# Kernel tuning notes

Hardware: AMD Instinct MI355X
Metric: run time of the kernel (lower is better)

The kernel has to match this reference:

```python
import jax, jax.numpy as jnp
import numpy as np

T = 5       # fixed temporal factor in the original forward
HEADS = 8
DIM = 512
DIM_HEAD = 64
INNER = HEADS * DIM_HEAD  # 512 (must equal DIM for the masked scatter)


def setup_inputs() -> dict:
    key = jax.random.key(0)
    ks = jax.random.split(key, 8)
    bt, n = 40, 3137  # b=8, t=5; n-1 = 56*56 visual tokens
    x = jax.random.normal(ks[0], (bt, n, DIM), dtype=jnp.float32)
    mask = jax.random.randint(ks[1], (bt, 56, 56), 0, 2).astype(jnp.float32)
    s = 1.0 / np.sqrt(DIM)
    w_vq = jax.random.normal(ks[2], (DIM, INNER), dtype=jnp.float32) * s
    w_vkv = jax.random.normal(ks[3], (DIM, 2 * INNER), dtype=jnp.float32) * s
    w_aqkv = jax.random.normal(ks[4], (DIM, 3 * INNER), dtype=jnp.float32) * s
    w_out = jax.random.normal(ks[5], (INNER, DIM), dtype=jnp.float32) * s
    b_out = jnp.zeros((DIM,), dtype=jnp.float32)
    return {"x": x, "mask": mask, "w_vq": w_vq, "w_vkv": w_vkv,
            "w_aqkv": w_aqkv, "w_out": w_out, "b_out": b_out}


def reference(x, mask, w_vq, w_vkv, w_aqkv, w_out, b_out):
    bt, n, dim = x.shape
    b = bt // T
    nv = n - 1
    dh = DIM_HEAD
    scale = dh ** -0.5

    A = x[:, 0]        # (bt, dim) -- single 'action' token per frame
    V = x[:, 1:]       # (bt, nv, dim)
    m = mask.reshape(bt, nv, 1)

    aq, ak, av = jnp.split(A @ w_aqkv, 3, axis=-1)      # each (bt, INNER)
    vk, vv = jnp.split(V @ w_vkv, 2, axis=-1)           # each (bt, nv, INNER)
    vq = V @ w_vq                                        # (bt, nv, INNER)

    # --- A -> V cross attention: per batch, T A-queries over T*nv V keys ---
    qa = aq.reshape(b, T, HEADS, dh)
    Kv = vk.reshape(b, T * nv, HEADS, dh)
    Vv = vv.reshape(b, T * nv, HEADS, dh)
    av_dots = jnp.einsum('bqhd,bkhd->bhqk', qa, Kv) * scale
    av_attn = jax.nn.softmax(av_dots, axis=-1)
    av_o = jnp.einsum('bhqk,bkhd->bqhd', av_attn, Vv)   # (b, T, H, dh)
    a_out = av_o.reshape(bt, 1, INNER)

    # --- V -> A cross attention with block mask: every V token attends only
    # to its own batch's T A-tokens (the -inf block fill in the original) ---
    Qv = vq.reshape(b, T, nv, HEADS, dh)
    Ka = ak.reshape(b, T, HEADS, dh)
    Va = av.reshape(b, T, HEADS, dh)
    va_dots = jnp.einsum('bfnhd,bkhd->bhfnk', Qv, Ka) * scale
    va_attn = jax.nn.softmax(va_dots, axis=-1)          # softmax over T keys
    va_o = jnp.einsum('bhfnk,bkhd->bfnhd', va_attn, Va)
    v_full = va_o.reshape(bt, nv, INNER)

    # original: scatter attn out into V.clone() then * mask, under no_grad()
    # => masked positions get attention output, others V*0 = 0; detached.
    v_out = jax.lax.stop_gradient(v_full * m)

    out = jnp.concatenate([a_out, v_out], axis=1)       # (bt, n, INNER)
    return out @ w_out + b_out
```

## Files before the change

kernel.cpp:

```cpp
#include <hip/hip_runtime.h>

typedef unsigned short u16;
typedef unsigned int u32;
typedef __attribute__((ext_vector_type(8))) u16 u16x8;
typedef __attribute__((ext_vector_type(8))) __bf16 bf16x8;
typedef __attribute__((ext_vector_type(4))) float f32x4;

__device__ __forceinline__ float b2f(u16 u){ return __uint_as_float(((u32)u)<<16); }
__device__ __forceinline__ u16 f2b(float f){
  u32 b = __float_as_uint(f);
  return (u16)((b + 0x7fffu + ((b>>16)&1u))>>16);
}
__device__ __forceinline__ void gload16(const void* g, void* l){
  __builtin_amdgcn_global_load_lds((__attribute__((address_space(1))) void*)g,
                                   (__attribute__((address_space(3))) void*)l, 16, 0, 0);
}
__device__ __forceinline__ float wred_max(float v){
#pragma unroll
  for (int o=32;o>0;o>>=1) v = fmaxf(v, __shfl_xor(v,o));
  return v;
}
__device__ __forceinline__ float wred_sum(float v){
#pragma unroll
  for (int o=32;o>0;o>>=1) v += __shfl_xor(v,o);
  return v;
}


__global__ void k_pre(const float* __restrict__ x, const float* __restrict__ wvq,
                      const float* __restrict__ wvkv, const float* __restrict__ wout,
                      const float* __restrict__ waqkv,
                      u16* __restrict__ xb, u16* __restrict__ W1T,
                      u16* __restrict__ WoutT, float* __restrict__ aqkv){
  const int bid = blockIdx.x, tid = threadIdx.x;
  if (bid < 2048){
    const int stride = 2048*256;
    for (int i = bid*256 + tid; i < 8030720; i += stride){
      const float4* p = (const float4*)(x + (size_t)i*8);
      float4 a = p[0], b = p[1];
      u16x8 o;
      o[0]=f2b(a.x); o[1]=f2b(a.y); o[2]=f2b(a.z); o[3]=f2b(a.w);
      o[4]=f2b(b.x); o[5]=f2b(b.y); o[6]=f2b(b.z); o[7]=f2b(b.w);
      *(u16x8*)(xb + (size_t)i*8) = o;
    }
  } else if (bid < 6144){
    int id = (bid-2048)*256 + tid;
    if (id < 786432){
      int n = id >> 9, k = id & 511;
      float v;
      if (n < 512){
        v = wvq[k*512 + n];
      } else {
        int j = n - 512, h = j >> 7, r = j & 127;
        int c2 = (r < 64) ? (h*64 + r) : (512 + h*64 + (r - 64));
        v = wvkv[k*1024 + c2];
      }
      W1T[id] = f2b(v);
    } else {
      int j = id - 786432;
      int n = j >> 9, k = j & 511;
      WoutT[j] = f2b(wout[k*512 + n]);
    }
  } else {
    int id = (bid-6144)*256 + tid;
    int bt = id / 1536, c = id % 1536;
    const float* xr = x + (size_t)bt*3137*512;
    float s = 0.f;
    for (int k=0;k<512;k++) s += xr[k]*waqkv[k*1536+c];
    aqkv[id] = s;
  }
}

template<int FOUT>
__global__ __launch_bounds__(512, 2) void k_gemm256(
    const u16* __restrict__ A, const u16* __restrict__ BT,
    int M, int N, int K, int NX,
    u16* __restrict__ Cb, float* __restrict__ Cf, const float* __restrict__ bias)
{
  __shared__ __align__(16) char Ls[4][32768];
  const int tid = threadIdx.x;
  const int wid = tid >> 6, lane = tid & 63;
  const int nwg = gridDim.x, orig = blockIdx.x;
  const int q8 = nwg >> 3, r8 = nwg & 7;
  const int xc = orig & 7, sl = orig >> 3;
  const int work = (xc < r8 ? xc*(q8+1) : r8*(q8+1) + (xc-r8)*q8) + sl;
  const int m0 = (work / NX) * 256, n0 = (work % NX) * 256;
  const size_t K2 = (size_t)K * 2;
  const char* Ab = (const char*)A;
  const char* Bb = (const char*)BT;
  size_t asrc[2], bsrc[2];
  const int ad0 = wid*1024, ad1 = 8192 + wid*1024;
#pragma unroll
  for (int i=0;i<2;i++){
    int row = (i*8 + wid)*16 + (lane & 15);
    int koff = (lane >> 4) << 4;
    int ra = m0 + row; if (ra >= M) ra = M - 1;
    asrc[i] = (size_t)ra * K2 + koff;
    bsrc[i] = (size_t)(n0 + row) * K2 + koff;
  }
#define STAGE(s4, ks) { \
    size_t ko = (size_t)(ks) * 64; \
    gload16(Ab + asrc[0] + ko, Ls[s4] + ad0); \
    gload16(Ab + asrc[1] + ko, Ls[s4] + ad1); \
    gload16(Bb + bsrc[0] + ko, Ls[s4] + 16384 + ad0); \
    gload16(Bb + bsrc[1] + ko, Ls[s4] + 16384 + ad1); }

  f32x4 acc[8][4] = {};
  const int awb = (wid >> 2) * 8192;
  const int bwb = 16384 + (wid & 3) * 4096;
  const int NS = K >> 5;
  STAGE(0,0) STAGE(1,1) STAGE(2,2)
  for (int s = 0; s < NS; ++s){
    if (s + 2 < NS)      { asm volatile("s_waitcnt vmcnt(8)" ::: "memory"); }
    else if (s + 1 < NS) { asm volatile("s_waitcnt vmcnt(4)" ::: "memory"); }
    else                 { asm volatile("s_waitcnt vmcnt(0)" ::: "memory"); }
    __builtin_amdgcn_s_barrier();
    __builtin_amdgcn_sched_barrier(0);
    if (s + 3 < NS) STAGE((s+3)&3, s+3)
    const char* base = Ls[s & 3];
    bf16x8 af[8], bfr[4];
#pragma unroll
    for (int i=0;i<4;i++) af[i]  = *(const bf16x8*)(base + awb + i*1024 + lane*16);
#pragma unroll
    for (int i=0;i<4;i++) bfr[i] = *(const bf16x8*)(base + bwb + i*1024 + lane*16);
    asm volatile("s_waitcnt lgkmcnt(0)" ::: "memory");
    __builtin_amdgcn_sched_barrier(0);
    __builtin_amdgcn_s_setprio(1);
#pragma unroll
    for (int mr=0;mr<4;mr++)
#pragma unroll
      for (int nc=0;nc<4;nc++)
        acc[mr][nc] = __builtin_amdgcn_mfma_f32_16x16x32_bf16(af[mr], bfr[nc], acc[mr][nc], 0,0,0);
    __builtin_amdgcn_s_setprio(0);
#pragma unroll
    for (int i=4;i<8;i++) af[i] = *(const bf16x8*)(base + awb + i*1024 + lane*16);
    asm volatile("s_waitcnt lgkmcnt(0)" ::: "memory");
    __builtin_amdgcn_sched_barrier(0);
    __builtin_amdgcn_s_setprio(1);
#pragma unroll
    for (int mr=4;mr<8;mr++)
#pragma unroll
      for (int nc=0;nc<4;nc++)
        acc[mr][nc] = __builtin_amdgcn_mfma_f32_16x16x32_bf16(af[mr], bfr[nc], acc[mr][nc], 0,0,0);
    __builtin_amdgcn_s_setprio(0);
  }
#undef STAGE
  const int wm = (wid >> 2) * 128, wn = (wid & 3) * 64;
  if (m0 + 256 <= M){
#pragma unroll
    for (int mr=0;mr<8;mr++){
#pragma unroll
      for (int nc=0;nc<4;nc++){
#pragma unroll
        for (int rg=0;rg<4;rg++){
          int row = m0 + wm + mr*16 + ((lane>>4)<<2) + rg;
          int col = n0 + wn + nc*16 + (lane&15);
          float v = acc[mr][nc][rg];
          if (FOUT) Cf[(size_t)row*N + col] = v + bias[col];
          else      Cb[(size_t)row*N + col] = f2b(v);
        }
      }
    }
  } else {
#pragma unroll
    for (int mr=0;mr<8;mr++){
#pragma unroll
      for (int nc=0;nc<4;nc++){
#pragma unroll
        for (int rg=0;rg<4;rg++){
          int row = m0 + wm + mr*16 + ((lane>>4)<<2) + rg;
          int col = n0 + wn + nc*16 + (lane&15);
          if (row < M){
            float v = acc[mr][nc][rg];
            if (FOUT) Cf[(size_t)row*N + col] = v + bias[col];
            else      Cb[(size_t)row*N + col] = f2b(v);
          }
        }
      }
    }
  }
}

__global__ __launch_bounds__(320) void k_attn_agent(
    const u16* __restrict__ out1, const float* __restrict__ aqkv,
    float* __restrict__ pm, float* __restrict__ pl, float* __restrict__ pacc)
{
  __shared__ __align__(16) char Ksm[16384];
  __shared__ __align__(16) char Vsm[16384];
  const int bid = blockIdx.x;
  const int sp = bid & 15, bh = bid >> 4, b = bh >> 3, h = bh & 7;
  const int tid = threadIdx.x, wid = tid >> 6, lane = tid & 63;
  const int q = wid;
  float qreg[64];
  {
    const float* ap = aqkv + ((size_t)(b*5+q)*1536 + h*64);
#pragma unroll
    for (int d=0; d<64; d++) qreg[d] = ap[d];
  }
  float m = -1e30f, l = 0.f;
  float acc[8] = {0,0,0,0,0,0,0,0};
  const int g0 = sp * 980;
  for (int c = 0; c < 8; c++){
    for (int idx = tid; idx < 2048; idx += 320){
      int r = idx >> 4, g = idx & 15;
      int loc = c*128 + r; if (loc > 979) loc = 979;
      int gk = g0 + loc;
      int tk = gk / 3136, nv = gk - tk*3136;
      size_t grow = (size_t)((b*5+tk)*3137 + 1 + nv)*1536 + 512 + h*128 + g*8;
      u16x8 v = *(const u16x8*)(out1 + grow);
      char* dst = (g < 8) ? Ksm : Vsm;
      int seg = g & 7;
      *(u16x8*)(dst + r*128 + ((seg*16) ^ ((r&7)<<4))) = v;
    }
    __syncthreads();
    float s0 = 0.f, s1 = 0.f;
#pragma unroll
    for (int seg=0; seg<8; seg++){
      const int r0 = lane, r1 = 64 + lane;
      u16x8 k0 = *(const u16x8*)(Ksm + r0*128 + ((seg*16) ^ ((r0&7)<<4)));
      u16x8 k1 = *(const u16x8*)(Ksm + r1*128 + ((seg*16) ^ ((r1&7)<<4)));
#pragma unroll
      for (int j=0;j<8;j++){
        s0 += qreg[seg*8+j]*b2f(k0[j]);
        s1 += qreg[seg*8+j]*b2f(k1[j]);
      }
    }
    s0 *= 0.125f; s1 *= 0.125f;
    const int locbase = c*128;
    if (locbase + lane >= 980)      s0 = -1e30f;
    if (locbase + 64 + lane >= 980) s1 = -1e30f;
    float cmax = wred_max(fmaxf(s0, s1));
    float mn = fmaxf(m, cmax);
    float resc = __expf(m - mn);
    float p0 = (s0 > -1e29f) ? __expf(s0 - mn) : 0.f;
    float p1 = (s1 > -1e29f) ? __expf(s1 - mn) : 0.f;
    l = l*resc + wred_sum(p0 + p1);
#pragma unroll
    for (int j=0;j<8;j++) acc[j] *= resc;
    const int g = lane >> 3, cc = lane & 7;
#pragma unroll
    for (int i=0;i<16;i++){
      int k = i*8 + g;
      u16x8 vv = *(const u16x8*)(Vsm + k*128 + ((cc*16) ^ ((k&7)<<4)));
      float p = (i < 8) ? __shfl(p0, k) : __shfl(p1, k-64);
#pragma unroll
      for (int j=0;j<8;j++) acc[j] += p*b2f(vv[j]);
    }
    m = mn;
    __syncthreads();
  }
#pragma unroll
  for (int j=0;j<8;j++){
    float v = acc[j];
    v += __shfl_xor(v, 8); v += __shfl_xor(v, 16); v += __shfl_xor(v, 32);
    acc[j] = v;
  }
  const int base = (bh*16 + sp)*5 + q;
  if (lane == 0){ pm[base] = m; pl[base] = l; }
  if (lane < 8){
    float* pa = pacc + (size_t)base*64 + lane*8;
#pragma unroll
    for (int j=0;j<8;j++) pa[j] = acc[j];
  }
}

__global__ __launch_bounds__(256) void k_attn_frame(
    const u16* __restrict__ out1, const float* __restrict__ aqkv,
    const float* __restrict__ mask, const float* __restrict__ pm,
    const float* __restrict__ pl, const float* __restrict__ pacc,
    u16* __restrict__ IN)
{
  const int bid = blockIdx.x, tid = threadIdx.x;
  if (bid < 3920){
    __shared__ float Ka[5][8][68];
    __shared__ float Va[5][8][68];
    const int b = bid / 490, bx = bid % 490;
    for (int i = tid; i < 2560; i += 256){
      int t = i >> 9, rem = i & 511, hh = rem >> 6, d = rem & 63;
      const float* src = aqkv + (size_t)(b*5+t)*1536;
      Ka[t][hh][d] = src[512 + hh*64 + d];
      Va[t][hh][d] = src[1024 + hh*64 + d];
    }
    __syncthreads();
    const int task = bx*256 + tid;
    const int h = task & 7, rl = task >> 3;
    const int f = rl / 3136, nv = rl - f*3136;
    const int bt = b*5 + f;
    const size_t r1 = (size_t)bt*3137 + 1 + nv;
    const u16* qp = out1 + r1*1536 + h*64;
    float qf[64];
#pragma unroll
    for (int sg=0; sg<8; sg++){
      u16x8 v = *(const u16x8*)(qp + sg*8);
#pragma unroll
      for (int j=0;j<8;j++) qf[sg*8+j] = b2f(v[j]);
    }
    float sd[5];
#pragma unroll
    for (int t=0;t<5;t++){
      float s = 0.f;
#pragma unroll
      for (int d=0;d<64;d++) s += qf[d]*Ka[t][h][d];
      sd[t] = s*0.125f;
    }
    float mx = sd[0];
#pragma unroll
    for (int t=1;t<5;t++) mx = fmaxf(mx, sd[t]);
    float p[5], ps = 0.f;
#pragma unroll
    for (int t=0;t<5;t++){ p[t] = __expf(sd[t]-mx); ps += p[t]; }
    const float mv = mask[(size_t)bt*3136 + nv] / ps;
    u16* op = IN + r1*512 + h*64;
#pragma unroll
    for (int sg=0; sg<8; sg++){
      u16x8 o;
#pragma unroll
      for (int j=0;j<8;j++){
        const int d = sg*8+j;
        float v = 0.f;
#pragma unroll
        for (int t=0;t<5;t++) v += p[t]*Va[t][h][d];
        o[j] = f2b(v*mv);
      }
      *(u16x8*)(op + sg*8) = o;
    }
  } else {
    const int id = (bid - 3920)*4 + (tid >> 6);
    const int d = tid & 63;
    const int q = id % 5, t2 = id / 5;
    const int h = t2 & 7, b = t2 >> 3;
    const int bh = b*8 + h;
    float ms = -1e30f;
#pragma unroll
    for (int s2=0;s2<16;s2++) ms = fmaxf(ms, pm[(bh*16+s2)*5+q]);
    float L = 0.f, o = 0.f;
#pragma unroll
    for (int s2=0;s2<16;s2++){
      int base = (bh*16+s2)*5+q;
      float w = __expf(pm[base]-ms);
      L += w*pl[base];
      o += w*pacc[(size_t)base*64 + d];
    }
    IN[(size_t)(b*5+q)*3137*512 + h*64 + d] = f2b(o / L);
  }
}

extern "C" void kernel_launch(void* const* d_in, const int* in_sizes, int n_in,
                              void* d_out, int out_size, void* d_ws, size_t ws_size,
                              hipStream_t stream)
{
  const float* x      = (const float*)d_in[0];
  const float* mask   = (const float*)d_in[1];
  const float* w_vq   = (const float*)d_in[2];
  const float* w_vkv  = (const float*)d_in[3];
  const float* w_aqkv = (const float*)d_in[4];
  const float* w_out  = (const float*)d_in[5];
  const float* b_out  = (const float*)d_in[6];
  float* out = (float*)d_out;
  char* ws = (char*)d_ws;

  constexpr size_t MR = 125480;
  constexpr size_t OFF_XB   = 0;
  constexpr size_t OFF_OUT1 = OFF_XB + MR*512*2;
  constexpr size_t OFF_W1T  = OFF_OUT1 + MR*1536*2;
  constexpr size_t OFF_WOT  = OFF_W1T + 1536*512*2;
  constexpr size_t OFF_AQKV = OFF_WOT + 512*512*2;
  constexpr size_t OFF_PM   = OFF_AQKV + 40*1536*4;
  constexpr size_t OFF_PL   = OFF_PM + 5120*4;
  constexpr size_t OFF_PACC = OFF_PL + 5120*4;

  u16* Xb     = (u16*)(ws + OFF_XB);
  u16* out1   = (u16*)(ws + OFF_OUT1);
  u16* W1T    = (u16*)(ws + OFF_W1T);
  u16* WoutT  = (u16*)(ws + OFF_WOT);
  float* aqkv = (float*)(ws + OFF_AQKV);
  float* pm   = (float*)(ws + OFF_PM);
  float* pl   = (float*)(ws + OFF_PL);
  float* pacc = (float*)(ws + OFF_PACC);

  k_pre<<<6384, 256, 0, stream>>>(x, w_vq, w_vkv, w_out, w_aqkv, Xb, W1T, WoutT, aqkv);
  k_gemm256<0><<<2946, 512, 0, stream>>>(Xb, W1T, (int)MR, 1536, 512, 6,
                                         out1, nullptr, nullptr);
  k_attn_agent<<<1024, 320, 0, stream>>>(out1, aqkv, pm, pl, pacc);
  k_attn_frame<<<4000, 256, 0, stream>>>(out1, aqkv, mask, pm, pl, pacc, Xb);
  k_gemm256<1><<<982, 512, 0, stream>>>(Xb, WoutT, (int)MR, 512, 512, 2,
                                        nullptr, out, b_out);
}
```

Baseline: 784.3 us.

## Merge agent and frame attention kernels, skip masked-out tokens, split combine

Fuses the A->V split-KV attention blocks and the per-token V->A frame attention blocks into one launch so the two independent workloads run concurrently, with a separate small kernel doing the split-softmax combine afterwards. The frame path now checks the mask first and writes zeros for masked-out tokens without loading Q or computing the softmax. This drops half the Q reads and compute on random masks, but adds a launch and makes the frame blocks use 320 threads and 32KB shared memory, which may lower occupancy.

```diff
diff --git a/kernel.cpp b/kernel.cpp
--- a/kernel.cpp
+++ b/kernel.cpp
@@ -181,168 +181,175 @@
   }
 }
 
-__global__ __launch_bounds__(320) void k_attn_agent(
+__global__ __launch_bounds__(320) void k_attn(
     const u16* __restrict__ out1, const float* __restrict__ aqkv,
-    float* __restrict__ pm, float* __restrict__ pl, float* __restrict__ pacc)
-{
-  __shared__ __align__(16) char Ksm[16384];
-  __shared__ __align__(16) char Vsm[16384];
-  const int bid = blockIdx.x;
-  const int sp = bid & 15, bh = bid >> 4, b = bh >> 3, h = bh & 7;
-  const int tid = threadIdx.x, wid = tid >> 6, lane = tid & 63;
-  const int q = wid;
-  float qreg[64];
-  {
-    const float* ap = aqkv + ((size_t)(b*5+q)*1536 + h*64);
-#pragma unroll
-    for (int d=0; d<64; d++) qreg[d] = ap[d];
-  }
-  float m = -1e30f, l = 0.f;
-  float acc[8] = {0,0,0,0,0,0,0,0};
-  const int g0 = sp * 980;
-  for (int c = 0; c < 8; c++){
-    for (int idx = tid; idx < 2048; idx += 320){
-      int r = idx >> 4, g = idx & 15;
-      int loc = c*128 + r; if (loc > 979) loc = 979;
-      int gk = g0 + loc;
-      int tk = gk / 3136, nv = gk - tk*3136;
-      size_t grow = (size_t)((b*5+tk)*3137 + 1 + nv)*1536 + 512 + h*128 + g*8;
-      u16x8 v = *(const u16x8*)(out1 + grow);
-      char* dst = (g < 8) ? Ksm : Vsm;
-      int seg = g & 7;
-      *(u16x8*)(dst + r*128 + ((seg*16) ^ ((r&7)<<4))) = v;
-    }
-    __syncthreads();
-    float s0 = 0.f, s1 = 0.f;
-#pragma unroll
-    for (int seg=0; seg<8; seg++){
-      const int r0 = lane, r1 = 64 + lane;
-      u16x8 k0 = *(const u16x8*)(Ksm + r0*128 + ((seg*16) ^ ((r0&7)<<4)));
-      u16x8 k1 = *(const u16x8*)(Ksm + r1*128 + ((seg*16) ^ ((r1&7)<<4)));
-#pragma unroll
-      for (int j=0;j<8;j++){
-        s0 += qreg[seg*8+j]*b2f(k0[j]);
-        s1 += qreg[seg*8+j]*b2f(k1[j]);
-      }
-    }
-    s0 *= 0.125f; s1 *= 0.125f;
-    const int locbase = c*128;
-    if (locbase + lane >= 980)      s0 = -1e30f;
-    if (locbase + 64 + lane >= 980) s1 = -1e30f;
-    float cmax = wred_max(fmaxf(s0, s1));
-    float mn = fmaxf(m, cmax);
-    float resc = __expf(m - mn);
-    float p0 = (s0 > -1e29f) ? __expf(s0 - mn) : 0.f;
-    float p1 = (s1 > -1e29f) ? __expf(s1 - mn) : 0.f;
-    l = l*resc + wred_sum(p0 + p1);
-#pragma unroll
-    for (int j=0;j<8;j++) acc[j] *= resc;
-    const int g = lane >> 3, cc = lane & 7;
-#pragma unroll
-    for (int i=0;i<16;i++){
-      int k = i*8 + g;
-      u16x8 vv = *(const u16x8*)(Vsm + k*128 + ((cc*16) ^ ((k&7)<<4)));
-      float p = (i < 8) ? __shfl(p0, k) : __shfl(p1, k-64);
-#pragma unroll
-      for (int j=0;j<8;j++) acc[j] += p*b2f(vv[j]);
-    }
-    m = mn;
-    __syncthreads();
-  }
-#pragma unroll
-  for (int j=0;j<8;j++){
-    float v = acc[j];
-    v += __shfl_xor(v, 8); v += __shfl_xor(v, 16); v += __shfl_xor(v, 32);
-    acc[j] = v;
-  }
-  const int base = (bh*16 + sp)*5 + q;
-  if (lane == 0){ pm[base] = m; pl[base] = l; }
-  if (lane < 8){
-    float* pa = pacc + (size_t)base*64 + lane*8;
-#pragma unroll
-    for (int j=0;j<8;j++) pa[j] = acc[j];
-  }
-}
-
-__global__ __launch_bounds__(256) void k_attn_frame(
-    const u16* __restrict__ out1, const float* __restrict__ aqkv,
-    const float* __restrict__ mask, const float* __restrict__ pm,
-    const float* __restrict__ pl, const float* __restrict__ pacc,
+    const float* __restrict__ mask,
+    float* __restrict__ pm, float* __restrict__ pl, float* __restrict__ pacc,
     u16* __restrict__ IN)
 {
+  __shared__ __align__(16) char smem[32768];
   const int bid = blockIdx.x, tid = threadIdx.x;
-  if (bid < 3920){
-    __shared__ float Ka[5][8][68];
-    __shared__ float Va[5][8][68];
-    const int b = bid / 490, bx = bid % 490;
-    for (int i = tid; i < 2560; i += 256){
+  if (bid < 1024){
+    char* Ksm = smem;
+    char* Vsm = smem + 16384;
+    const int sp = bid & 15, bh = bid >> 4, b = bh >> 3, h = bh & 7;
+    const int wid = tid >> 6, lane = tid & 63;
+    const int q = wid;
+    float qreg[64];
+    {
+      const float* ap = aqkv + ((size_t)(b*5+q)*1536 + h*64);
+#pragma unroll
+      for (int d=0; d<64; d++) qreg[d] = ap[d];
+    }
+    float m = -1e30f, l = 0.f;
+    float acc[8] = {0,0,0,0,0,0,0,0};
+    const int g0 = sp * 980;
+    for (int c = 0; c < 8; c++){
+      for (int idx = tid; idx < 2048; idx += 320){
+        int r = idx >> 4, g = idx & 15;
+        int loc = c*128 + r; if (loc > 979) loc = 979;
+        int gk = g0 + loc;
+        int tk = gk / 3136, nv = gk - tk*3136;
+        size_t grow = (size_t)((b*5+tk)*3137 + 1 + nv)*1536 + 512 + h*128 + g*8;
+        u16x8 v = *(const u16x8*)(out1 + grow);
+        char* dst = (g < 8) ? Ksm : Vsm;
+        int seg = g & 7;
+        *(u16x8*)(dst + r*128 + ((seg*16) ^ ((r&7)<<4))) = v;
+      }
+      __syncthreads();
+      float s0 = 0.f, s1 = 0.f;
+#pragma unroll
+      for (int seg=0; seg<8; seg++){
+        const int r0 = lane, r1 = 64 + lane;
+        u16x8 k0 = *(const u16x8*)(Ksm + r0*128 + ((seg*16) ^ ((r0&7)<<4)));
+        u16x8 k1 = *(const u16x8*)(Ksm + r1*128 + ((seg*16) ^ ((r1&7)<<4)));
+#pragma unroll
+        for (int j=0;j<8;j++){
+          s0 += qreg[seg*8+j]*b2f(k0[j]);
+          s1 += qreg[seg*8+j]*b2f(k1[j]);
+        }
+      }
+      s0 *= 0.125f; s1 *= 0.125f;
+      const int locbase = c*128;
+      if (locbase + lane >= 980)      s0 = -1e30f;
+      if (locbase + 64 + lane >= 980) s1 = -1e30f;
+      float cmax = wred_max(fmaxf(s0, s1));
+      float mn = fmaxf(m, cmax);
+      float resc = __expf(m - mn);
+      float p0 = (s0 > -1e29f) ? __expf(s0 - mn) : 0.f;
+      float p1 = (s1 > -1e29f) ? __expf(s1 - mn) : 0.f;
+      l = l*resc + wred_sum(p0 + p1);
+#pragma unroll
+      for (int j=0;j<8;j++) acc[j] *= resc;
+      const int g = lane >> 3, cc = lane & 7;
+#pragma unroll
+      for (int i=0;i<16;i++){
+        int k = i*8 + g;
+        u16x8 vv = *(const u16x8*)(Vsm + k*128 + ((cc*16) ^ ((k&7)<<4)));
+        float p = (i < 8) ? __shfl(p0, k) : __shfl(p1, k-64);
+#pragma unroll
+        for (int j=0;j<8;j++) acc[j] += p*b2f(vv[j]);
+      }
+      m = mn;
+      __syncthreads();
+    }
+#pragma unroll
+    for (int j=0;j<8;j++){
+      float v = acc[j];
+      v += __shfl_xor(v, 8); v += __shfl_xor(v, 16); v += __shfl_xor(v, 32);
+      acc[j] = v;
+    }
+    const int base = (bh*16 + sp)*5 + q;
+    if (lane == 0){ pm[base] = m; pl[base] = l; }
+    if (lane < 8){
+      float* pa = pacc + (size_t)base*64 + lane*8;
+#pragma unroll
+      for (int j=0;j<8;j++) pa[j] = acc[j];
+    }
+  } else {
+    float (*Ka)[8][68] = (float(*)[8][68])smem;
+    float (*Va)[8][68] = (float(*)[8][68])(smem + 10880);
+    const int fid = bid - 1024;
+    const int b = fid / 392, bx = fid % 392;
+    for (int i = tid; i < 2560; i += 320){
       int t = i >> 9, rem = i & 511, hh = rem >> 6, d = rem & 63;
       const float* src = aqkv + (size_t)(b*5+t)*1536;
       Ka[t][hh][d] = src[512 + hh*64 + d];
       Va[t][hh][d] = src[1024 + hh*64 + d];
     }
     __syncthreads();
-    const int task = bx*256 + tid;
+    const int task = bx*320 + tid;
     const int h = task & 7, rl = task >> 3;
     const int f = rl / 3136, nv = rl - f*3136;
     const int bt = b*5 + f;
     const size_t r1 = (size_t)bt*3137 + 1 + nv;
-    const u16* qp = out1 + r1*1536 + h*64;
-    float qf[64];
-#pragma unroll
-    for (int sg=0; sg<8; sg++){
-      u16x8 v = *(const u16x8*)(qp + sg*8);
-#pragma unroll
-      for (int j=0;j<8;j++) qf[sg*8+j] = b2f(v[j]);
-    }
-    float sd[5];
-#pragma unroll
-    for (int t=0;t<5;t++){
-      float s = 0.f;
-#pragma unroll
-      for (int d=0;d<64;d++) s += qf[d]*Ka[t][h][d];
-      sd[t] = s*0.125f;
-    }
-    float mx = sd[0];
-#pragma unroll
-    for (int t=1;t<5;t++) mx = fmaxf(mx, sd[t]);
-    float p[5], ps = 0.f;
-#pragma unroll
-    for (int t=0;t<5;t++){ p[t] = __expf(sd[t]-mx); ps += p[t]; }
-    const float mv = mask[(size_t)bt*3136 + nv] / ps;
     u16* op = IN + r1*512 + h*64;
-#pragma unroll
-    for (int sg=0; sg<8; sg++){
-      u16x8 o;
-#pragma unroll
-      for (int j=0;j<8;j++){
-        const int d = sg*8+j;
-        float v = 0.f;
-#pragma unroll
-        for (int t=0;t<5;t++) v += p[t]*Va[t][h][d];
-        o[j] = f2b(v*mv);
-      }
-      *(u16x8*)(op + sg*8) = o;
-    }
-  } else {
-    const int id = (bid - 3920)*4 + (tid >> 6);
-    const int d = tid & 63;
-    const int q = id % 5, t2 = id / 5;
-    const int h = t2 & 7, b = t2 >> 3;
-    const int bh = b*8 + h;
-    float ms = -1e30f;
-#pragma unroll
-    for (int s2=0;s2<16;s2++) ms = fmaxf(ms, pm[(bh*16+s2)*5+q]);
-    float L = 0.f, o = 0.f;
-#pragma unroll
-    for (int s2=0;s2<16;s2++){
-      int base = (bh*16+s2)*5+q;
-      float w = __expf(pm[base]-ms);
-      L += w*pl[base];
-      o += w*pacc[(size_t)base*64 + d];
-    }
-    IN[(size_t)(b*5+q)*3137*512 + h*64 + d] = f2b(o / L);
-  }
+    const float mraw = mask[(size_t)bt*3136 + nv];
+    if (mraw == 0.f){
+      u16x8 z = {};
+#pragma unroll
+      for (int sg=0; sg<8; sg++) *(u16x8*)(op + sg*8) = z;
+    } else {
+      const u16* qp = out1 + r1*1536 + h*64;
+      float qf[64];
+#pragma unroll
+      for (int sg=0; sg<8; sg++){
+        u16x8 v = *(const u16x8*)(qp + sg*8);
+#pragma unroll
+        for (int j=0;j<8;j++) qf[sg*8+j] = b2f(v[j]);
+      }
+      float sd[5];
+#pragma unroll
+      for (int t=0;t<5;t++){
+        float s = 0.f;
+#pragma unroll
+        for (int d=0;d<64;d++) s += qf[d]*Ka[t][h][d];
+        sd[t] = s*0.125f;
+      }
+      float mx = sd[0];
+#pragma unroll
+      for (int t=1;t<5;t++) mx = fmaxf(mx, sd[t]);
+      float p[5], ps = 0.f;
+#pragma unroll
+      for (int t=0;t<5;t++){ p[t] = __expf(sd[t]-mx); ps += p[t]; }
+      const float mv = mraw / ps;
+#pragma unroll
+      for (int sg=0; sg<8; sg++){
+        u16x8 o;
+#pragma unroll
+        for (int j=0;j<8;j++){
+          const int d = sg*8+j;
+          float v = 0.f;
+#pragma unroll
+          for (int t=0;t<5;t++) v += p[t]*Va[t][h][d];
+          o[j] = f2b(v*mv);
+        }
+        *(u16x8*)(op + sg*8) = o;
+      }
+    }
+  }
+}
+
+__global__ void k_combine(const float* __restrict__ pm, const float* __restrict__ pl,
+                          const float* __restrict__ pacc, u16* __restrict__ IN)
+{
+  const int id = blockIdx.x;
+  const int q = id % 5, t2 = id / 5;
+  const int h = t2 & 7, b = t2 >> 3;
+  const int d = threadIdx.x;
+  const int bh = b*8 + h;
+  float ms = -1e30f;
+#pragma unroll
+  for (int s2=0;s2<16;s2++) ms = fmaxf(ms, pm[(bh*16+s2)*5+q]);
+  float L = 0.f, o = 0.f;
+#pragma unroll
+  for (int s2=0;s2<16;s2++){
+    int base = (bh*16+s2)*5+q;
+    float w = __expf(pm[base]-ms);
+    L += w*pl[base];
+    o += w*pacc[(size_t)base*64 + d];
+  }
+  IN[(size_t)(b*5+q)*3137*512 + h*64 + d] = f2b(o / L);
 }
 
 extern "C" void kernel_launch(void* const* d_in, const int* in_sizes, int n_in,
@@ -381,8 +388,8 @@
   k_pre<<<6384, 256, 0, stream>>>(x, w_vq, w_vkv, w_out, w_aqkv, Xb, W1T, WoutT, aqkv);
   k_gemm256<0><<<2946, 512, 0, stream>>>(Xb, W1T, (int)MR, 1536, 512, 6,
                                          out1, nullptr, nullptr);
-  k_attn_agent<<<1024, 320, 0, stream>>>(out1, aqkv, pm, pl, pacc);
-  k_attn_frame<<<4000, 256, 0, stream>>>(out1, aqkv, mask, pm, pl, pacc, Xb);
+  k_attn<<<4160, 320, 0, stream>>>(out1, aqkv, mask, pm, pl, pacc, Xb);
+  k_combine<<<320, 64, 0, stream>>>(pm, pl, pacc, Xb);
   k_gemm256<1><<<982, 512, 0, stream>>>(Xb, WoutT, (int)MR, 512, 512, 2,
                                         nullptr, out, b_out);
 }
```

Measured after the change: 785.0 us. No clear change (+0.1%).
